# Performance work log

Measured on AMD Instinct MI355X. Metric: run time of the kernel, lower is better.

## Reference

```python
import jax, jax.numpy as jnp
import numpy as np

B, L, K, H = 256, 256, 128, 256


def setup_inputs() -> dict:
    key = jax.random.key(0)
    ks = jax.random.split(key, 24)

    def u(k, shape, fan):
        s = 1.0 / np.sqrt(fan)
        return jax.random.uniform(k, shape, minval=-s, maxval=s, dtype=jnp.float32)

    x = jax.random.normal(ks[0], (B, L, K), jnp.float32)
    mask = (jax.random.uniform(ks[1], (B, L, K)) < 0.7).astype(jnp.float32)
    record_num = jax.random.randint(ks[2], (B,), L // 2, L + 1)
    ts = jnp.cumsum(jax.random.uniform(ks[3], (B, L), minval=0.1, maxval=1.0, dtype=jnp.float32), axis=1)
    time_stamp = ts * (jnp.arange(L)[None, :] < record_num[:, None]).astype(jnp.float32)

    return {
        "x": x,
        "mask": mask,
        "time_stamp": time_stamp,
        # TemporalDecay h: W [H,K], stdv = 1/sqrt(out)=1/sqrt(H)
        "W_gh": u(ks[4], (H, K), H), "b_gh": u(ks[5], (H,), H),
        # TemporalDecay x (diag): W [K,K], stdv = 1/sqrt(K)
        "W_gx": u(ks[6], (K, K), K), "b_gx": u(ks[7], (K,), K),
        # hist_reg: Linear(H -> K), stdv = 1/sqrt(H)
        "W_hist": u(ks[8], (K, H), H), "b_hist": u(ks[9], (K,), H),
        "W_feat": u(ks[10], (K, K), K), "b_feat": u(ks[11], (K,), K),
        # weight_combine: Linear(2K -> K), stdv = 1/sqrt(2K)
        "W_comb": u(ks[12], (K, 2 * K), 2 * K), "b_comb": u(ks[13], (K,), 2 * K),
        # GRUCell(2K -> H): uniform 1/sqrt(H)
        "W_ih": u(ks[14], (3 * H, 2 * K), H), "W_hh": u(ks[15], (3 * H, H), H),
        "b_ih": u(ks[16], (3 * H,), H), "b_hh": u(ks[17], (3 * H,), H),
        # out: Linear(H -> 1)
        "W_out": u(ks[18], (1, H), H), "b_out": u(ks[19], (1,), H),
        "record_num": record_num,
        "direct": 0,
    }


def _forward(x, mask, time_stamp, W_gh, b_gh, W_gx, b_gx, W_hist, b_hist,
             W_feat, b_feat, W_comb, b_comb, W_ih, W_hh, b_ih, b_hh,
             W_out, b_out, record_num):
    Bs, Ls, Ks = x.shape
    Hs = W_gh.shape[0]
    eye = jnp.eye(Ks, dtype=x.dtype)
    W_gx_m = W_gx * eye                 # diag temporal decay
    W_feat_m = W_feat * (1.0 - eye)

    # --- deltas (gen_aux_data): d[0]=1; d[t] = |ts[t]-ts[t-1]| + (1-m[t])*d[t-1] ---
    gaps = jnp.abs(jnp.diff(time_stamp, axis=1))          # [B, L-1]
    mask_t = jnp.swapaxes(mask, 0, 1)                     # [L, B, K]

    def dstep(prev, inp):
        gap, m = inp                                      # [B], [B,K]
        d = gap[:, None] + (1.0 - m) * prev
        return d, d

    d0 = jnp.ones((Bs, Ks), x.dtype)
    _, drest = jax.lax.scan(dstep, d0, (gaps.T, mask_t[1:]))
    deltas = jnp.concatenate([d0[None], drest], axis=0)   # [L, B, K]
    valid = (jnp.arange(Ls)[:, None] < record_num[None, :])  # break at record_num
    deltas = jnp.where(valid[:, :, None], deltas, 0.0)

    evals = (time_stamp != 0).astype(x.dtype)             # [B, L]

    x_t = jnp.swapaxes(x, 0, 1)                           # [L, B, K]
    e_t = evals.T                                         # [L, B]

    def step(carry, inp):
        h, xloss = carry
        xt, mt, dt, et = inp                              # [B,K],[B,K],[B,K],[B]
        e_m = et[:, None]
        gamma_h = jnp.exp(-jax.nn.relu(dt @ W_gh.T + b_gh))   # [B,H]
        gamma_x = jnp.exp(-jax.nn.relu(dt @ W_gx_m.T + b_gx)) # [B,K]
        h_prev = h
        h = h * gamma_h
        x_h = h @ W_hist.T + b_hist
        msum = jnp.sum(mt) + 1e-5
        xloss = xloss + jnp.sum(jnp.abs(xt - x_h) * mt) / msum
        x_c = mt * xt + (1.0 - mt) * x_h
        z_h = x_c @ W_feat_m.T + b_feat
        xloss = xloss + jnp.sum(jnp.abs(xt - z_h) * mt * e_m) / msum
        alpha = jnp.concatenate([gamma_x, mt], axis=1) @ W_comb.T + b_comb
        c_h = alpha * z_h + (1.0 - alpha) * x_h
        xloss = xloss + jnp.sum(jnp.abs(xt - c_h) * mt * e_m) / msum
        c_c = mt * xt + (1.0 - mt) * c_h
        inputs = jnp.concatenate([c_c, mt], axis=1)           # [B, 2K]
        gi = inputs @ W_ih.T + b_ih                           # [B, 3H]
        gh = h @ W_hh.T + b_hh
        ir, iz, ig = jnp.split(gi, 3, axis=1)
        hr, hz, hg = jnp.split(gh, 3, axis=1)
        r = jax.nn.sigmoid(ir + hr)
        z = jax.nn.sigmoid(iz + hz)
        n = jnp.tanh(ig + r * hg)
        h_new = (1.0 - z) * n + z * h
        h_new = h_new * e_m + (1.0 - e_m) * h_prev            # freeze h past record
        return (h_new, xloss), c_c * e_m

    h0 = jnp.zeros((Bs, Hs), x.dtype)
    (h_fin, x_loss), imps = jax.lax.scan(step, (h0, jnp.float32(0.0)), (x_t, mask_t, deltas, e_t))
    imputations = jnp.swapaxes(imps, 0, 1)                # [B, L, K]
    predictions = jax.nn.sigmoid(h_fin @ W_out.T + b_out) # [B, 1]
    return imputations, x_loss, predictions


def reference(x, mask, time_stamp, W_gh, b_gh, W_gx, b_gx, W_hist, b_hist,
              W_feat, b_feat, W_comb, b_comb, W_ih, W_hh, b_ih, b_hh,
              W_out, b_out, record_num, direct):
    return _forward(x, mask, time_stamp, W_gh, b_gh, W_gx, b_gx, W_hist, b_hist,
                    W_feat, b_feat, W_comb, b_comb, W_ih, W_hh, b_ih, b_hh,
                    W_out, b_out, record_num)
```

## Files before the change

kernel.cpp:

```cpp
#include <hip/hip_runtime.h>
#include <math.h>

#define BT 256
#define LT 256
#define KT 128
#define HT 256
#define LOSS_IDX ((size_t)BT*LT*KT)
#define PRED_IDX (LOSS_IDX + 1)
#define LDP 1280
#define GH0 0
#define AL0 256
#define GI0 384
#define ZP0 1152

typedef _Float16 h2 __attribute__((ext_vector_type(2)));
typedef _Float16 f16x8 __attribute__((ext_vector_type(8)));
typedef float f32x4 __attribute__((ext_vector_type(4)));

__device__ __forceinline__ float fd2(h2 a, h2 b, float c){
#if __has_builtin(__builtin_amdgcn_fdot2)
  return __builtin_amdgcn_fdot2(a, b, c, false);
#else
  return c + (float)a[0]*(float)b[0] + (float)a[1]*(float)b[1];
#endif
}
__device__ __forceinline__ float dot8(f16x8 w, f16x8 a, float acc){
  acc = fd2(__builtin_shufflevector(w,w,0,1), __builtin_shufflevector(a,a,0,1), acc);
  acc = fd2(__builtin_shufflevector(w,w,2,3), __builtin_shufflevector(a,a,2,3), acc);
  acc = fd2(__builtin_shufflevector(w,w,4,5), __builtin_shufflevector(a,a,4,5), acc);
  acc = fd2(__builtin_shufflevector(w,w,6,7), __builtin_shufflevector(a,a,6,7), acc);
  return acc;
}
__device__ __forceinline__ float sigf(float v){ return 1.0f/(1.0f + __expf(-v)); }
__device__ __forceinline__ float tanh_fast(float v){
  float a = fminf(fabsf(v), 15.0f);
  float e2 = __expf(2.0f*a);
  float r = (e2 - 1.0f)/(e2 + 1.0f);
  return copysignf(r, v);
}
__device__ __forceinline__ float f16bits(unsigned u, int hi){
  union { unsigned short s; _Float16 h; } c;
  c.s = (unsigned short)(hi ? (u >> 16) : (u & 0xffff));
  return (float)c.h;
}

__global__ void pack_cast(const float* __restrict__ src, _Float16* __restrict__ dst,
                          int J, int Kd, int diag, int total){
  int idx = blockIdx.x*256 + threadIdx.x;
  if (idx >= total) return;
  float v = src[idx];
  if (diag && (idx / Kd) == (idx % Kd)) v = 0.0f;
  dst[idx] = (_Float16)v;
}
__global__ void pack_rowchunks(const float* __restrict__ src, _Float16* __restrict__ dst,
                               int J, int K, int total){
  int idx = blockIdx.x*256 + threadIdx.x;
  if (idx >= total) return;
  int j = idx % J, c = idx / J;
  #pragma unroll
  for (int e = 0; e < 8; ++e)
    dst[(size_t)idx*8 + e] = (_Float16)src[(size_t)j*K + c*8 + e];
}
__global__ void pack_col(const float* __restrict__ src, _Float16* __restrict__ dst,
                         int J, int Kc, int ld, int diag, int total){
  int idx = blockIdx.x*256 + threadIdx.x;
  if (idx >= total) return;
  int j = idx % J, k = idx / J;
  float v = src[(size_t)j*ld + k];
  if (diag && j == k) v = 0.0f;
  dst[idx] = (_Float16)v;
}

__global__ __launch_bounds__(128) void scan_kernel(
    const float* __restrict__ x, const float* __restrict__ mask, const float* __restrict__ ts,
    const float* __restrict__ W_gx, const float* __restrict__ b_gx,
    const int* __restrict__ record_num,
    _Float16* __restrict__ deltas, _Float16* __restrict__ Agx, _Float16* __restrict__ U)
{
  int b = blockIdx.x, k = threadIdx.x;
  int rn = record_num[b];
  float gxd = W_gx[(size_t)k*KT + k];
  float bgx = b_gx[k];
  float d = 1.0f, tsp = 0.0f;
  for (int t0 = 0; t0 < LT; t0 += 8){
    float xv[8], mv[8], tsv[8];
    #pragma unroll
    for (int u = 0; u < 8; ++u){
      size_t off = ((size_t)b*LT + t0 + u)*KT + k;
      xv[u] = x[off]; mv[u] = mask[off];
      tsv[u] = ts[(size_t)b*LT + t0 + u];
    }
    #pragma unroll
    for (int u = 0; u < 8; ++u){
      int t = t0 + u;
      if (t > 0){
        float gap = fabsf(tsv[u] - (u ? tsv[u-1] : tsp));
        d = gap + (1.0f - mv[u])*d;
      }
      float e = (t < rn) ? 1.0f : 0.0f;
      float dev = d * e;
      size_t row = (size_t)b*LT + t;
      deltas[row*KT + k] = (_Float16)dev;
      float gx = __expf(-fmaxf(fmaf(dev, gxd, bgx), 0.0f));
      Agx[row*2*KT + k]      = (_Float16)gx;
      Agx[row*2*KT + KT + k] = (_Float16)mv[u];
      U[row*2*KT + k]        = (_Float16)(mv[u]*xv[u]);
      U[row*2*KT + KT + k]   = (_Float16)mv[u];
    }
    tsp = tsv[7];
  }
}

__global__ void msum_kernel(const float* __restrict__ mask, float* __restrict__ msumInv){
  __shared__ float red[256];
  int t = blockIdx.x;
  float acc = 0.0f;
  for (int i = threadIdx.x; i < BT*KT; i += 256){
    int b = i >> 7, k = i & 127;
    acc += mask[((size_t)b*LT + t)*KT + k];
  }
  red[threadIdx.x] = acc; __syncthreads();
  for (int s = 128; s > 0; s >>= 1){
    if (threadIdx.x < s) red[threadIdx.x] += red[threadIdx.x + s];
    __syncthreads();
  }
  if (threadIdx.x == 0) msumInv[t] = 1.0f/(red[0] + 1e-5f);
}

__global__ __launch_bounds__(256) void gemm_f16(
    const _Float16* __restrict__ A, long ldA, int K,
    const _Float16* __restrict__ B, long ldB,
    _Float16* __restrict__ C, long colofs,
    const float* __restrict__ bias, int op)
{
  const int w = threadIdx.x >> 6, lane = threadIdx.x & 63;
  const int ml = lane & 15, quad = lane >> 4;
  const long m0 = (long)blockIdx.x*64 + w*16;
  const long nb0 = (long)blockIdx.y*64;
  f32x4 acc[4] = {{0,0,0,0},{0,0,0,0},{0,0,0,0},{0,0,0,0}};
  for (int kc = 0; kc < K; kc += 32){
    f16x8 a = *(const f16x8*)(A + (m0 + ml)*ldA + kc + quad*8);
    #pragma unroll
    for (int nt = 0; nt < 4; ++nt){
      f16x8 bfr = *(const f16x8*)(B + (nb0 + nt*16 + ml)*ldB + kc + quad*8);
      acc[nt] = __builtin_amdgcn_mfma_f32_16x16x32_f16(a, bfr, acc[nt], 0, 0, 0);
    }
  }
  #pragma unroll
  for (int nt = 0; nt < 4; ++nt){
    long col = nb0 + nt*16 + ml;
    float bv = (op >= 1) ? bias[col] : 0.0f;
    #pragma unroll
    for (int r = 0; r < 4; ++r){
      float v = acc[nt][r];
      if (op >= 1) v += bv;
      if (op == 2) v = __expf(-fmaxf(v, 0.0f));
      long row = m0 + quad*4 + r;
      C[row*LDP + colofs + col] = (_Float16)v;
    }
  }
}

#define NT 768

struct __align__(16) SeqS {
  f16x8 whist_l[32*128];
  _Float16 wfc_l[128*128];
  float h[HT];
  float hs[HT];
  alignas(16) _Float16 hsh[HT];
  float gh[3*HT];
  float gi[3*HT];
  float xh[KT];
  float part6[6][KT];
  float v3[KT], v5[KT];
  int lidx[136];
  int posk[KT];
  int cnt;
  unsigned pb[2][LDP/2];
  float xb[2][KT], mb[2][KT];
  float bhist[KT], bfeat[KT];
  float bhh[3*HT];
  float wout[HT];
  float minv[LT];
  float red[NT/64];
};

__global__ __launch_bounds__(NT, 1) void rits_seq(
    const float* __restrict__ x, const float* __restrict__ mask,
    const int* __restrict__ record_num, const float* __restrict__ msumInv,
    const _Float16* __restrict__ P,
    const f16x8* __restrict__ Whh_p, const f16x8* __restrict__ Whist_p,
    const _Float16* __restrict__ Wfc, const _Float16* __restrict__ Wihc,
    const float* __restrict__ b_hist, const float* __restrict__ b_feat,
    const float* __restrict__ b_hh,
    const float* __restrict__ W_out, const float* __restrict__ b_out,
    float* __restrict__ out)
{
  __shared__ SeqS s;
  const int tid = threadIdx.x;
  const int b = blockIdx.x;
  const int rn = record_num[b];
  const unsigned* __restrict__ Pd = (const unsigned*)P + (size_t)b*LT*(LDP/2);

  for (int i = tid; i < 32*128; i += NT) s.whist_l[i] = Whist_p[i];
  for (int i = tid; i < 128*128/2; i += NT)
    ((unsigned*)s.wfc_l)[i] = ((const unsigned*)Wfc)[i];
  if (tid < HT) s.h[tid] = 0.0f;
  if (tid < KT){ s.bhist[tid] = b_hist[tid]; s.bfeat[tid] = b_feat[tid]; }
  if (tid < 3*HT) s.bhh[tid] = b_hh[tid];
  if (tid < 136) s.lidx[tid] = 0;
  if (tid >= 256 && tid < 512) s.wout[tid - 256] = W_out[tid - 256];
  if (tid >= 512 && tid < 512 + LT) s.minv[tid - 512] = msumInv[tid - 512];
  if (tid < LDP/2) s.pb[0][tid] = Pd[tid];
  else if (tid < LDP/2 + KT){
    int k = tid - LDP/2;
    s.xb[0][k] = x[((size_t)b*LT)*KT + k];
    s.mb[0][k] = mask[((size_t)b*LT)*KT + k];
  }
  __syncthreads();

  float loss = 0.0f;

  for (int t = 0; t < LT; ++t){
    const int cur = t & 1, nxt = cur ^ 1;

    unsigned pr0 = 0; float prx = 0.0f, prm = 0.0f;
    if (t < LT - 1){
      if (tid < LDP/2) pr0 = Pd[(size_t)(t+1)*(LDP/2) + tid];
      else {
        int k = tid - LDP/2;
        size_t offx = ((size_t)b*LT + t + 1)*KT + k;
        prx = x[offx]; prm = mask[offx];
      }
    }
    if (tid == 0) s.cnt = 0;
    if (tid < HT){
      float g = f16bits(s.pb[cur][tid >> 1], tid & 1);
      float hsv = s.h[tid] * g;
      s.hs[tid] = hsv;
      s.hsh[tid] = (_Float16)hsv;
    }
    __syncthreads();

    {
      const f16x8* hp = (const f16x8*)s.hsh;
      if (tid < KT){
        float a2 = 0.0f;
        #pragma unroll 8
        for (int c = 0; c < 32; ++c)
          a2 = dot8(s.whist_l[c*128 + tid], hp[c], a2);
        float xh = a2 + s.bhist[tid];
        s.xh[tid] = xh;
        float mv = s.mb[cur][tid], xv = s.xb[cur][tid];
        loss += fabsf(xv - xh) * mv * s.minv[t];
        if (mv == 0.0f){
          int pp = atomicAdd(&s.cnt, 1);
          s.lidx[pp] = tid; s.v3[pp] = xh; s.posk[tid] = pp;
        }
      }
      float acc = 0.0f;
      #pragma unroll 8
      for (int c = 0; c < 32; ++c)
        acc = dot8(Whh_p[c*768 + tid], hp[c], acc);
      s.gh[tid] = acc;
    }
    __syncthreads();

    const int c0 = s.cnt;
    const int c4 = (c0 + 7) & ~7;
    {
      int st = tid >> 7, j = tid & 127;
      float a = 0.0f;
      for (int i = st; i < c0; i += 6)
        a += s.v3[i] * (float)s.wfc_l[s.lidx[i]*128 + j];
      s.part6[st][j] = a;
    }
    float wpre[16];
    #pragma unroll
    for (int u = 0; u < 16; ++u)
      wpre[u] = (u < c4) ? (float)Wihc[(size_t)s.lidx[u]*768 + tid] : 0.0f;
    __syncthreads();

    if (tid < KT){
      const int j = tid;
      if (j >= c0 && j < c4) s.v5[j] = 0.0f;
      float z = f16bits(s.pb[cur][ZP0/2 + (j >> 1)], j & 1) + s.bfeat[j]
              + s.part6[0][j] + s.part6[1][j] + s.part6[2][j]
              + s.part6[3][j] + s.part6[4][j] + s.part6[5][j];
      float al = f16bits(s.pb[cur][AL0/2 + (j >> 1)], j & 1);
      float xh = s.xh[j];
      float mv = s.mb[cur][j], xv = s.xb[cur][j];
      float e = (t < rn) ? 1.0f : 0.0f;
      float inv = s.minv[t];
      float ch = al*z + (1.0f - al)*xh;
      loss += (fabsf(xv - z) + fabsf(xv - ch)) * mv * e * inv;
      float cc = mv*xv + (1.0f - mv)*ch;
      out[((size_t)b*LT + t)*KT + j] = cc * e;
      if (mv == 0.0f) s.v5[s.posk[j]] = ch;
    }
    __syncthreads();

    {
      float g = f16bits(s.pb[cur][GI0/2 + (tid >> 1)], tid & 1);
      #pragma unroll
      for (int u = 0; u < 16; ++u)
        if (u < c4) g += s.v5[u] * wpre[u];
      for (int i = 16; i < c4; i += 8){
        #pragma unroll
        for (int u = 0; u < 8; ++u)
          g += s.v5[i + u] * (float)Wihc[(size_t)s.lidx[i + u]*768 + tid];
      }
      s.gi[tid] = g;
    }
    __syncthreads();

    if (tid < HT){
      const int j = tid;
      float ir = s.gi[j], iz = s.gi[HT + j], ig = s.gi[2*HT + j];
      float hr = s.gh[j] + s.bhh[j];
      float hz = s.gh[HT + j] + s.bhh[HT + j];
      float hg = s.gh[2*HT + j] + s.bhh[2*HT + j];
      float r = sigf(ir + hr);
      float zg = sigf(iz + hz);
      float n = tanh_fast(ig + r*hg);
      float hn = (1.0f - zg)*n + zg*s.hs[j];
      if (t < rn) s.h[j] = hn;
    }
    if (t < LT - 1){
      if (tid < LDP/2) s.pb[nxt][tid] = pr0;
      else {
        int k = tid - LDP/2;
        s.xb[nxt][k] = prx; s.mb[nxt][k] = prm;
      }
    }
    __syncthreads();
  }

  #pragma unroll
  for (int off = 32; off; off >>= 1) loss += __shfl_down(loss, off);
  if ((tid & 63) == 0) s.red[tid >> 6] = loss;
  __syncthreads();
  if (tid == 0){
    float tot = 0.0f;
    #pragma unroll
    for (int w = 0; w < NT/64; ++w) tot += s.red[w];
    atomicAdd(&out[LOSS_IDX], tot);
  }

  if (tid < HT) s.gh[tid] = s.h[tid] * s.wout[tid];
  __syncthreads();
  for (int st2 = 128; st2 > 0; st2 >>= 1){
    if (tid < st2) s.gh[tid] += s.gh[tid + st2];
    __syncthreads();
  }
  if (tid == 0) out[PRED_IDX + b] = sigf(s.gh[0] + b_out[0]);
}

extern "C" void kernel_launch(void* const* d_in, const int* in_sizes, int n_in,
                              void* d_out, int out_size, void* d_ws, size_t ws_size,
                              hipStream_t stream){
  const float* x      = (const float*)d_in[0];
  const float* mask   = (const float*)d_in[1];
  const float* ts     = (const float*)d_in[2];
  const float* W_gh   = (const float*)d_in[3];
  const float* b_gh   = (const float*)d_in[4];
  const float* W_gx   = (const float*)d_in[5];
  const float* b_gx   = (const float*)d_in[6];
  const float* W_hist = (const float*)d_in[7];
  const float* b_hist = (const float*)d_in[8];
  const float* W_feat = (const float*)d_in[9];
  const float* b_feat = (const float*)d_in[10];
  const float* W_comb = (const float*)d_in[11];
  const float* b_comb = (const float*)d_in[12];
  const float* W_ih   = (const float*)d_in[13];
  const float* W_hh   = (const float*)d_in[14];
  const float* b_ih   = (const float*)d_in[15];
  const float* b_hh   = (const float*)d_in[16];
  const float* W_out  = (const float*)d_in[17];
  const float* b_out  = (const float*)d_in[18];
  const int*   rn     = (const int*)d_in[19];
  float* out = (float*)d_out;
  char* ws = (char*)d_ws;

  size_t off = 0;
  auto alloc = [&](size_t bytes) -> char* {
    char* p = ws + off;
    off += (bytes + 255) & ~(size_t)255;
    return p;
  };
  _Float16* P      = (_Float16*)alloc((size_t)BT*LT*LDP*2);
  _Float16* deltas = (_Float16*)alloc((size_t)BT*LT*KT*2);
  _Float16* Agx    = (_Float16*)alloc((size_t)BT*LT*2*KT*2);
  _Float16* U      = (_Float16*)alloc((size_t)BT*LT*2*KT*2);
  _Float16* WghF   = (_Float16*)alloc(HT*KT*2);
  _Float16* WcombF = (_Float16*)alloc(KT*2*KT*2);
  _Float16* WihF   = (_Float16*)alloc(3*HT*2*KT*2);
  _Float16* WfeatF = (_Float16*)alloc(KT*KT*2);
  _Float16* Whh_p  = (_Float16*)alloc(3*HT*HT*2);
  _Float16* Whist_p= (_Float16*)alloc(KT*HT*2);
  _Float16* Wfc    = (_Float16*)alloc(KT*KT*2);
  _Float16* Wihc   = (_Float16*)alloc(KT*3*HT*2);
  float* msumInv   = (float*)alloc(LT*4);

  auto grid1 = [](int n){ return dim3((n + 255)/256); };
  pack_cast<<<grid1(HT*KT), 256, 0, stream>>>(W_gh, WghF, HT, KT, 0, HT*KT);
  pack_cast<<<grid1(KT*2*KT), 256, 0, stream>>>(W_comb, WcombF, KT, 2*KT, 0, KT*2*KT);
  pack_cast<<<grid1(3*HT*2*KT), 256, 0, stream>>>(W_ih, WihF, 3*HT, 2*KT, 0, 3*HT*2*KT);
  pack_cast<<<grid1(KT*KT), 256, 0, stream>>>(W_feat, WfeatF, KT, KT, 1, KT*KT);
  pack_rowchunks<<<grid1(3*HT*(HT/8)), 256, 0, stream>>>(W_hh, Whh_p, 3*HT, HT, 3*HT*(HT/8));
  pack_rowchunks<<<grid1(KT*(HT/8)), 256, 0, stream>>>(W_hist, Whist_p, KT, HT, KT*(HT/8));
  pack_col<<<grid1(KT*KT), 256, 0, stream>>>(W_feat, Wfc, KT, KT, KT, 1, KT*KT);
  pack_col<<<grid1(768*KT), 256, 0, stream>>>(W_ih, Wihc, 3*HT, KT, 2*KT, 0, 3*HT*KT);

  scan_kernel<<<dim3(BT), dim3(KT), 0, stream>>>(x, mask, ts, W_gx, b_gx, rn, deltas, Agx, U);
  msum_kernel<<<dim3(LT), dim3(256), 0, stream>>>(mask, msumInv);

  const int MR = BT*LT;
  gemm_f16<<<dim3(MR/64, HT/64), 256, 0, stream>>>(deltas, KT, KT, WghF, KT, P, GH0, b_gh, 2);
  gemm_f16<<<dim3(MR/64, KT/64), 256, 0, stream>>>(Agx, 2*KT, 2*KT, WcombF, 2*KT, P, AL0, b_comb, 1);
  gemm_f16<<<dim3(MR/64, 3*HT/64), 256, 0, stream>>>(U, 2*KT, 2*KT, WihF, 2*KT, P, GI0, b_ih, 1);
  gemm_f16<<<dim3(MR/64, KT/64), 256, 0, stream>>>(U, 2*KT, KT, WfeatF, KT, P, ZP0, (const float*)nullptr, 0);

  hipMemsetAsync((void*)(out + LOSS_IDX), 0, sizeof(float), stream);

  rits_seq<<<dim3(BT), dim3(NT), 0, stream>>>(x, mask, rn, msumInv, P,
      (const f16x8*)Whh_p, (const f16x8*)Whist_p, Wfc, Wihc,
      b_hist, b_feat, b_hh, W_out, b_out, out);
}
```

Baseline: 2.415 ms.

## Prefetch W_hh rows into registers and split dot-product accumulators

Loads most of each thread's W_hh column slice from global memory into registers at the top of each timestep, before the first barrier, so the fetch overlaps the h-scaling work. The rest is loaded after the barrier. Both the recurrent and history-regression dot products now use four independent accumulators to break the serial FMA dependency chain. The gathered W_ih loads in the input-gate loop are software-pipelined one batch ahead. The scaled hidden state stays in a register instead of shared memory. This raises register pressure, with 32 f16x8 vectors live per thread at 768 threads per block, which risks spilling or lower occupancy.

```diff
diff --git a/kernel.cpp b/kernel.cpp
--- a/kernel.cpp
+++ b/kernel.cpp
@@ -162,12 +162,13 @@
 }
 
 #define NT 768
+#define WHPRE 24
+#define WHINL (32 - WHPRE)
 
 struct __align__(16) SeqS {
   f16x8 whist_l[32*128];
   _Float16 wfc_l[128*128];
   float h[HT];
-  float hs[HT];
   alignas(16) _Float16 hsh[HT];
   float gh[3*HT];
   float gi[3*HT];
@@ -225,6 +226,9 @@
   for (int t = 0; t < LT; ++t){
     const int cur = t & 1, nxt = cur ^ 1;
 
+    f16x8 wA[WHPRE];
+    #pragma unroll
+    for (int c = 0; c < WHPRE; ++c) wA[c] = Whh_p[c*768 + tid];
     unsigned pr0 = 0; float prx = 0.0f, prm = 0.0f;
     if (t < LT - 1){
       if (tid < LDP/2) pr0 = Pd[(size_t)(t+1)*(LDP/2) + tid];
@@ -235,22 +239,45 @@
       }
     }
     if (tid == 0) s.cnt = 0;
+    float hs_r = 0.0f;
     if (tid < HT){
       float g = f16bits(s.pb[cur][tid >> 1], tid & 1);
-      float hsv = s.h[tid] * g;
-      s.hs[tid] = hsv;
-      s.hsh[tid] = (_Float16)hsv;
+      hs_r = s.h[tid] * g;
+      s.hsh[tid] = (_Float16)hs_r;
     }
     __syncthreads();
 
     {
       const f16x8* hp = (const f16x8*)s.hsh;
+      f16x8 wB[WHINL];
+      #pragma unroll
+      for (int c = 0; c < WHINL; ++c) wB[c] = Whh_p[(WHPRE + c)*768 + tid];
+      float acc0 = 0.0f, acc1 = 0.0f, acc2 = 0.0f, acc3 = 0.0f;
+      #pragma unroll
+      for (int c = 0; c < WHPRE; c += 4){
+        acc0 = dot8(wA[c],   hp[c],   acc0);
+        acc1 = dot8(wA[c+1], hp[c+1], acc1);
+        acc2 = dot8(wA[c+2], hp[c+2], acc2);
+        acc3 = dot8(wA[c+3], hp[c+3], acc3);
+      }
+      #pragma unroll
+      for (int c = 0; c < WHINL; c += 4){
+        acc0 = dot8(wB[c],   hp[WHPRE + c],   acc0);
+        acc1 = dot8(wB[c+1], hp[WHPRE + c+1], acc1);
+        acc2 = dot8(wB[c+2], hp[WHPRE + c+2], acc2);
+        acc3 = dot8(wB[c+3], hp[WHPRE + c+3], acc3);
+      }
+      s.gh[tid] = (acc0 + acc1) + (acc2 + acc3);
       if (tid < KT){
-        float a2 = 0.0f;
-        #pragma unroll 8
-        for (int c = 0; c < 32; ++c)
-          a2 = dot8(s.whist_l[c*128 + tid], hp[c], a2);
-        float xh = a2 + s.bhist[tid];
+        float a0 = 0.0f, a1 = 0.0f, a2 = 0.0f, a3 = 0.0f;
+        #pragma unroll
+        for (int c = 0; c < 32; c += 4){
+          a0 = dot8(s.whist_l[c*128 + tid],     hp[c],   a0);
+          a1 = dot8(s.whist_l[(c+1)*128 + tid], hp[c+1], a1);
+          a2 = dot8(s.whist_l[(c+2)*128 + tid], hp[c+2], a2);
+          a3 = dot8(s.whist_l[(c+3)*128 + tid], hp[c+3], a3);
+        }
+        float xh = (a0 + a1) + (a2 + a3) + s.bhist[tid];
         s.xh[tid] = xh;
         float mv = s.mb[cur][tid], xv = s.xb[cur][tid];
         loss += fabsf(xv - xh) * mv * s.minv[t];
@@ -259,11 +286,6 @@
           s.lidx[pp] = tid; s.v3[pp] = xh; s.posk[tid] = pp;
         }
       }
-      float acc = 0.0f;
-      #pragma unroll 8
-      for (int c = 0; c < 32; ++c)
-        acc = dot8(Whh_p[c*768 + tid], hp[c], acc);
-      s.gh[tid] = acc;
     }
     __syncthreads();
 
@@ -306,10 +328,24 @@
       #pragma unroll
       for (int u = 0; u < 16; ++u)
         if (u < c4) g += s.v5[u] * wpre[u];
-      for (int i = 16; i < c4; i += 8){
+      float wnx[8];
+      if (16 < c4){
         #pragma unroll
         for (int u = 0; u < 8; ++u)
-          g += s.v5[i + u] * (float)Wihc[(size_t)s.lidx[i + u]*768 + tid];
+          wnx[u] = (float)Wihc[(size_t)s.lidx[16 + u]*768 + tid];
+      }
+      for (int i = 16; i < c4; i += 8){
+        float wcu[8];
+        #pragma unroll
+        for (int u = 0; u < 8; ++u) wcu[u] = wnx[u];
+        if (i + 8 < c4){
+          #pragma unroll
+          for (int u = 0; u < 8; ++u)
+            wnx[u] = (float)Wihc[(size_t)s.lidx[i + 8 + u]*768 + tid];
+        }
+        #pragma unroll
+        for (int u = 0; u < 8; ++u)
+          g += s.v5[i + u] * wcu[u];
       }
       s.gi[tid] = g;
     }
@@ -324,7 +360,7 @@
       float r = sigf(ir + hr);
       float zg = sigf(iz + hz);
       float n = tanh_fast(ig + r*hg);
-      float hn = (1.0f - zg)*n + zg*s.hs[j];
+      float hn = (1.0f - zg)*n + zg*hs_r;
       if (t < rn) s.h[j] = hn;
     }
     if (t < LT - 1){
```

Result: slower. 4.647 ms (+92.4%).

## Process two batch sequences per workgroup to share recurrent weight loads

Applied to the files above, without the earlier changes.

Each workgroup now runs the recurrence for two batch elements at once, and the grid is halved. Each W_hh and W_hist chunk is loaded once and applied to both hidden states, halving recurrent-weight traffic per sequence. Idle thread groups now handle the second sequence's elementwise work. The cost is roughly double the per-step work on each workgroup, fewer prefetched W_ih columns (8 instead of 16 per sequence), and only half as many workgroups, which may leave many CUs unused on a 256-CU device.

```diff
diff --git a/kernel.cpp b/kernel.cpp
--- a/kernel.cpp
+++ b/kernel.cpp
@@ -166,19 +166,18 @@
 struct __align__(16) SeqS {
   f16x8 whist_l[32*128];
   _Float16 wfc_l[128*128];
-  float h[HT];
-  float hs[HT];
-  alignas(16) _Float16 hsh[HT];
-  float gh[3*HT];
-  float gi[3*HT];
-  float xh[KT];
-  float part6[6][KT];
-  float v3[KT], v5[KT];
-  int lidx[136];
-  int posk[KT];
-  int cnt;
-  unsigned pb[2][LDP/2];
-  float xb[2][KT], mb[2][KT];
+  float h0[HT], h1[HT];
+  alignas(16) _Float16 hsh0[HT], hsh1[HT];
+  float gh0[3*HT], gh1[3*HT];
+  float gi0[3*HT], gi1[3*HT];
+  float xh0[KT], xh1[KT];
+  float part0[3][KT], part1[3][KT];
+  float v30[KT], v50[KT], v31[KT], v51[KT];
+  int lidx0[136], lidx1[136];
+  int posk0[KT], posk1[KT];
+  int cnt0, cnt1;
+  unsigned pb0[2][LDP/2], pb1[2][LDP/2];
+  float xb0[2][KT], mb0[2][KT], xb1[2][KT], mb1[2][KT];
   float bhist[KT], bfeat[KT];
   float bhh[3*HT];
   float wout[HT];
@@ -199,24 +198,29 @@
 {
   __shared__ SeqS s;
   const int tid = threadIdx.x;
-  const int b = blockIdx.x;
-  const int rn = record_num[b];
-  const unsigned* __restrict__ Pd = (const unsigned*)P + (size_t)b*LT*(LDP/2);
+  const int b0 = blockIdx.x*2, b1 = b0 + 1;
+  const int rn0 = record_num[b0], rn1 = record_num[b1];
+  const unsigned* __restrict__ Pd0 = (const unsigned*)P + (size_t)b0*LT*(LDP/2);
+  const unsigned* __restrict__ Pd1 = (const unsigned*)P + (size_t)b1*LT*(LDP/2);
 
   for (int i = tid; i < 32*128; i += NT) s.whist_l[i] = Whist_p[i];
   for (int i = tid; i < 128*128/2; i += NT)
     ((unsigned*)s.wfc_l)[i] = ((const unsigned*)Wfc)[i];
-  if (tid < HT) s.h[tid] = 0.0f;
+  if (tid < HT){ s.h0[tid] = 0.0f; s.h1[tid] = 0.0f; }
   if (tid < KT){ s.bhist[tid] = b_hist[tid]; s.bfeat[tid] = b_feat[tid]; }
   if (tid < 3*HT) s.bhh[tid] = b_hh[tid];
-  if (tid < 136) s.lidx[tid] = 0;
+  if (tid < 136){ s.lidx0[tid] = 0; s.lidx1[tid] = 0; }
   if (tid >= 256 && tid < 512) s.wout[tid - 256] = W_out[tid - 256];
   if (tid >= 512 && tid < 512 + LT) s.minv[tid - 512] = msumInv[tid - 512];
-  if (tid < LDP/2) s.pb[0][tid] = Pd[tid];
-  else if (tid < LDP/2 + KT){
+  if (tid < LDP/2){
+    s.pb0[0][tid] = Pd0[tid];
+    s.pb1[0][tid] = Pd1[tid];
+  } else if (tid < LDP/2 + KT){
     int k = tid - LDP/2;
-    s.xb[0][k] = x[((size_t)b*LT)*KT + k];
-    s.mb[0][k] = mask[((size_t)b*LT)*KT + k];
+    s.xb0[0][k] = x[((size_t)b0*LT)*KT + k];
+    s.mb0[0][k] = mask[((size_t)b0*LT)*KT + k];
+    s.xb1[0][k] = x[((size_t)b1*LT)*KT + k];
+    s.mb1[0][k] = mask[((size_t)b1*LT)*KT + k];
   }
   __syncthreads();
 
@@ -225,113 +229,192 @@
   for (int t = 0; t < LT; ++t){
     const int cur = t & 1, nxt = cur ^ 1;
 
-    unsigned pr0 = 0; float prx = 0.0f, prm = 0.0f;
+    unsigned pra = 0, prb = 0;
+    float prx0 = 0.0f, prm0 = 0.0f, prx1 = 0.0f, prm1 = 0.0f;
     if (t < LT - 1){
-      if (tid < LDP/2) pr0 = Pd[(size_t)(t+1)*(LDP/2) + tid];
-      else {
+      if (tid < LDP/2){
+        pra = Pd0[(size_t)(t+1)*(LDP/2) + tid];
+        prb = Pd1[(size_t)(t+1)*(LDP/2) + tid];
+      } else {
         int k = tid - LDP/2;
-        size_t offx = ((size_t)b*LT + t + 1)*KT + k;
-        prx = x[offx]; prm = mask[offx];
-      }
-    }
-    if (tid == 0) s.cnt = 0;
+        size_t o0 = ((size_t)b0*LT + t + 1)*KT + k;
+        size_t o1 = ((size_t)b1*LT + t + 1)*KT + k;
+        prx0 = x[o0]; prm0 = mask[o0];
+        prx1 = x[o1]; prm1 = mask[o1];
+      }
+    }
+    if (tid == 0) s.cnt0 = 0;
+    if (tid == 1) s.cnt1 = 0;
+    float hs_r = 0.0f;
     if (tid < HT){
-      float g = f16bits(s.pb[cur][tid >> 1], tid & 1);
-      float hsv = s.h[tid] * g;
-      s.hs[tid] = hsv;
-      s.hsh[tid] = (_Float16)hsv;
+      float g = f16bits(s.pb0[cur][tid >> 1], tid & 1);
+      hs_r = s.h0[tid] * g;
+      s.hsh0[tid] = (_Float16)hs_r;
+    } else if (tid < 2*HT){
+      int j = tid - HT;
+      float g = f16bits(s.pb1[cur][j >> 1], j & 1);
+      hs_r = s.h1[j] * g;
+      s.hsh1[j] = (_Float16)hs_r;
     }
     __syncthreads();
 
     {
-      const f16x8* hp = (const f16x8*)s.hsh;
+      const f16x8* hp0 = (const f16x8*)s.hsh0;
+      const f16x8* hp1 = (const f16x8*)s.hsh1;
+      float g00 = 0.0f, g01 = 0.0f, g10 = 0.0f, g11 = 0.0f;
+      #pragma unroll 8
+      for (int c = 0; c < 32; c += 2){
+        f16x8 w0 = Whh_p[(size_t)c*768 + tid];
+        f16x8 w1 = Whh_p[(size_t)(c+1)*768 + tid];
+        g00 = dot8(w0, hp0[c],   g00);
+        g10 = dot8(w0, hp1[c],   g10);
+        g01 = dot8(w1, hp0[c+1], g01);
+        g11 = dot8(w1, hp1[c+1], g11);
+      }
+      s.gh0[tid] = g00 + g01;
+      s.gh1[tid] = g10 + g11;
       if (tid < KT){
-        float a2 = 0.0f;
+        float a00 = 0.0f, a01 = 0.0f, a10 = 0.0f, a11 = 0.0f;
         #pragma unroll 8
-        for (int c = 0; c < 32; ++c)
-          a2 = dot8(s.whist_l[c*128 + tid], hp[c], a2);
-        float xh = a2 + s.bhist[tid];
-        s.xh[tid] = xh;
-        float mv = s.mb[cur][tid], xv = s.xb[cur][tid];
-        loss += fabsf(xv - xh) * mv * s.minv[t];
-        if (mv == 0.0f){
-          int pp = atomicAdd(&s.cnt, 1);
-          s.lidx[pp] = tid; s.v3[pp] = xh; s.posk[tid] = pp;
+        for (int c = 0; c < 32; c += 2){
+          f16x8 w0 = s.whist_l[c*128 + tid];
+          f16x8 w1 = s.whist_l[(c+1)*128 + tid];
+          a00 = dot8(w0, hp0[c],   a00);
+          a10 = dot8(w0, hp1[c],   a10);
+          a01 = dot8(w1, hp0[c+1], a01);
+          a11 = dot8(w1, hp1[c+1], a11);
         }
-      }
-      float acc = 0.0f;
-      #pragma unroll 8
-      for (int c = 0; c < 32; ++c)
-        acc = dot8(Whh_p[c*768 + tid], hp[c], acc);
-      s.gh[tid] = acc;
-    }
-    __syncthreads();
-
-    const int c0 = s.cnt;
-    const int c4 = (c0 + 7) & ~7;
+        float xh0 = a00 + a01 + s.bhist[tid];
+        float xh1 = a10 + a11 + s.bhist[tid];
+        s.xh0[tid] = xh0; s.xh1[tid] = xh1;
+        float mv0 = s.mb0[cur][tid], xv0 = s.xb0[cur][tid];
+        float mv1 = s.mb1[cur][tid], xv1 = s.xb1[cur][tid];
+        loss += (fabsf(xv0 - xh0)*mv0 + fabsf(xv1 - xh1)*mv1) * s.minv[t];
+        if (mv0 == 0.0f){
+          int pp = atomicAdd(&s.cnt0, 1);
+          s.lidx0[pp] = tid; s.v30[pp] = xh0; s.posk0[tid] = pp;
+        }
+        if (mv1 == 0.0f){
+          int pp = atomicAdd(&s.cnt1, 1);
+          s.lidx1[pp] = tid; s.v31[pp] = xh1; s.posk1[tid] = pp;
+        }
+      }
+    }
+    __syncthreads();
+
+    const int c00 = s.cnt0, c01 = s.cnt1;
+    const int c40 = (c00 + 7) & ~7, c41 = (c01 + 7) & ~7;
     {
-      int st = tid >> 7, j = tid & 127;
-      float a = 0.0f;
-      for (int i = st; i < c0; i += 6)
-        a += s.v3[i] * (float)s.wfc_l[s.lidx[i]*128 + j];
-      s.part6[st][j] = a;
-    }
-    float wpre[16];
+      int sg = tid >> 7, j = tid & 127;
+      if (sg < 3){
+        float a = 0.0f;
+        for (int i = sg; i < c00; i += 3)
+          a += s.v30[i] * (float)s.wfc_l[s.lidx0[i]*128 + j];
+        s.part0[sg][j] = a;
+      } else {
+        int sg1 = sg - 3;
+        float a = 0.0f;
+        for (int i = sg1; i < c01; i += 3)
+          a += s.v31[i] * (float)s.wfc_l[s.lidx1[i]*128 + j];
+        s.part1[sg1][j] = a;
+      }
+    }
+    float wpre0[8], wpre1[8];
     #pragma unroll
-    for (int u = 0; u < 16; ++u)
-      wpre[u] = (u < c4) ? (float)Wihc[(size_t)s.lidx[u]*768 + tid] : 0.0f;
-    __syncthreads();
-
-    if (tid < KT){
-      const int j = tid;
-      if (j >= c0 && j < c4) s.v5[j] = 0.0f;
-      float z = f16bits(s.pb[cur][ZP0/2 + (j >> 1)], j & 1) + s.bfeat[j]
-              + s.part6[0][j] + s.part6[1][j] + s.part6[2][j]
-              + s.part6[3][j] + s.part6[4][j] + s.part6[5][j];
-      float al = f16bits(s.pb[cur][AL0/2 + (j >> 1)], j & 1);
-      float xh = s.xh[j];
-      float mv = s.mb[cur][j], xv = s.xb[cur][j];
-      float e = (t < rn) ? 1.0f : 0.0f;
-      float inv = s.minv[t];
-      float ch = al*z + (1.0f - al)*xh;
-      loss += (fabsf(xv - z) + fabsf(xv - ch)) * mv * e * inv;
-      float cc = mv*xv + (1.0f - mv)*ch;
-      out[((size_t)b*LT + t)*KT + j] = cc * e;
-      if (mv == 0.0f) s.v5[s.posk[j]] = ch;
+    for (int u = 0; u < 8; ++u){
+      wpre0[u] = (u < c40) ? (float)Wihc[(size_t)s.lidx0[u]*768 + tid] : 0.0f;
+      wpre1[u] = (u < c41) ? (float)Wihc[(size_t)s.lidx1[u]*768 + tid] : 0.0f;
+    }
+    __syncthreads();
+
+    if (tid < 2*KT){
+      const int j = tid & 127;
+      if (tid < KT){
+        if (j >= c00 && j < c40) s.v50[j] = 0.0f;
+        float z = f16bits(s.pb0[cur][ZP0/2 + (j >> 1)], j & 1) + s.bfeat[j]
+                + s.part0[0][j] + s.part0[1][j] + s.part0[2][j];
+        float al = f16bits(s.pb0[cur][AL0/2 + (j >> 1)], j & 1);
+        float xh = s.xh0[j];
+        float mv = s.mb0[cur][j], xv = s.xb0[cur][j];
+        float e = (t < rn0) ? 1.0f : 0.0f;
+        float inv = s.minv[t];
+        float ch = al*z + (1.0f - al)*xh;
+        loss += (fabsf(xv - z) + fabsf(xv - ch)) * mv * e * inv;
+        float cc = mv*xv + (1.0f - mv)*ch;
+        out[((size_t)b0*LT + t)*KT + j] = cc * e;
+        if (mv == 0.0f) s.v50[s.posk0[j]] = ch;
+      } else {
+        if (j >= c01 && j < c41) s.v51[j] = 0.0f;
+        float z = f16bits(s.pb1[cur][ZP0/2 + (j >> 1)], j & 1) + s.bfeat[j]
+                + s.part1[0][j] + s.part1[1][j] + s.part1[2][j];
+        float al = f16bits(s.pb1[cur][AL0/2 + (j >> 1)], j & 1);
+        float xh = s.xh1[j];
+        float mv = s.mb1[cur][j], xv = s.xb1[cur][j];
+        float e = (t < rn1) ? 1.0f : 0.0f;
+        float inv = s.minv[t];
+        float ch = al*z + (1.0f - al)*xh;
+        loss += (fabsf(xv - z) + fabsf(xv - ch)) * mv * e * inv;
+        float cc = mv*xv + (1.0f - mv)*ch;
+        out[((size_t)b1*LT + t)*KT + j] = cc * e;
+        if (mv == 0.0f) s.v51[s.posk1[j]] = ch;
+      }
     }
     __syncthreads();
 
     {
-      float g = f16bits(s.pb[cur][GI0/2 + (tid >> 1)], tid & 1);
+      float g0 = f16bits(s.pb0[cur][GI0/2 + (tid >> 1)], tid & 1);
+      float g1 = f16bits(s.pb1[cur][GI0/2 + (tid >> 1)], tid & 1);
       #pragma unroll
-      for (int u = 0; u < 16; ++u)
-        if (u < c4) g += s.v5[u] * wpre[u];
-      for (int i = 16; i < c4; i += 8){
+      for (int u = 0; u < 8; ++u){
+        if (u < c40) g0 += s.v50[u] * wpre0[u];
+        if (u < c41) g1 += s.v51[u] * wpre1[u];
+      }
+      for (int i = 8; i < c40; i += 8){
         #pragma unroll
         for (int u = 0; u < 8; ++u)
-          g += s.v5[i + u] * (float)Wihc[(size_t)s.lidx[i + u]*768 + tid];
-      }
-      s.gi[tid] = g;
+          g0 += s.v50[i + u] * (float)Wihc[(size_t)s.lidx0[i + u]*768 + tid];
+      }
+      for (int i = 8; i < c41; i += 8){
+        #pragma unroll
+        for (int u = 0; u < 8; ++u)
+          g1 += s.v51[i + u] * (float)Wihc[(size_t)s.lidx1[i + u]*768 + tid];
+      }
+      s.gi0[tid] = g0;
+      s.gi1[tid] = g1;
     }
     __syncthreads();
 
     if (tid < HT){
       const int j = tid;
-      float ir = s.gi[j], iz = s.gi[HT + j], ig = s.gi[2*HT + j];
-      float hr = s.gh[j] + s.bhh[j];
-      float hz = s.gh[HT + j] + s.bhh[HT + j];
-      float hg = s.gh[2*HT + j] + s.bhh[2*HT + j];
+      float ir = s.gi0[j], iz = s.gi0[HT + j], ig = s.gi0[2*HT + j];
+      float hr = s.gh0[j] + s.bhh[j];
+      float hz = s.gh0[HT + j] + s.bhh[HT + j];
+      float hg = s.gh0[2*HT + j] + s.bhh[2*HT + j];
       float r = sigf(ir + hr);
       float zg = sigf(iz + hz);
       float n = tanh_fast(ig + r*hg);
-      float hn = (1.0f - zg)*n + zg*s.hs[j];
-      if (t < rn) s.h[j] = hn;
+      float hn = (1.0f - zg)*n + zg*hs_r;
+      if (t < rn0) s.h0[j] = hn;
+    } else if (tid < 2*HT){
+      const int j = tid - HT;
+      float ir = s.gi1[j], iz = s.gi1[HT + j], ig = s.gi1[2*HT + j];
+      float hr = s.gh1[j] + s.bhh[j];
+      float hz = s.gh1[HT + j] + s.bhh[HT + j];
+      float hg = s.gh1[2*HT + j] + s.bhh[2*HT + j];
+      float r = sigf(ir + hr);
+      float zg = sigf(iz + hz);
+      float n = tanh_fast(ig + r*hg);
+      float hn = (1.0f - zg)*n + zg*hs_r;
+      if (t < rn1) s.h1[j] = hn;
     }
     if (t < LT - 1){
-      if (tid < LDP/2) s.pb[nxt][tid] = pr0;
-      else {
+      if (tid < LDP/2){
+        s.pb0[nxt][tid] = pra;
+        s.pb1[nxt][tid] = prb;
+      } else {
         int k = tid - LDP/2;
-        s.xb[nxt][k] = prx; s.mb[nxt][k] = prm;
+        s.xb0[nxt][k] = prx0; s.mb0[nxt][k] = prm0;
+        s.xb1[nxt][k] = prx1; s.mb1[nxt][k] = prm1;
       }
     }
     __syncthreads();
@@ -348,13 +431,16 @@
     atomicAdd(&out[LOSS_IDX], tot);
   }
 
-  if (tid < HT) s.gh[tid] = s.h[tid] * s.wout[tid];
+  if (tid < HT) s.gh0[tid] = s.h0[tid] * s.wout[tid];
+  else if (tid < 2*HT) s.gh1[tid - HT] = s.h1[tid - HT] * s.wout[tid - HT];
   __syncthreads();
   for (int st2 = 128; st2 > 0; st2 >>= 1){
-    if (tid < st2) s.gh[tid] += s.gh[tid + st2];
-    __syncthreads();
-  }
-  if (tid == 0) out[PRED_IDX + b] = sigf(s.gh[0] + b_out[0]);
+    if (tid < st2) s.gh0[tid] += s.gh0[tid + st2];
+    else if (tid >= 256 && tid < 256 + st2) s.gh1[tid - 256] += s.gh1[tid - 256 + st2];
+    __syncthreads();
+  }
+  if (tid == 0)   out[PRED_IDX + b0] = sigf(s.gh0[0] + b_out[0]);
+  if (tid == 256) out[PRED_IDX + b1] = sigf(s.gh1[0] + b_out[0]);
 }
 
 extern "C" void kernel_launch(void* const* d_in, const int* in_sizes, int n_in,
@@ -424,7 +510,7 @@
 
   hipMemsetAsync((void*)(out + LOSS_IDX), 0, sizeof(float), stream);
 
-  rits_seq<<<dim3(BT), dim3(NT), 0, stream>>>(x, mask, rn, msumInv, P,
+  rits_seq<<<dim3(BT/2), dim3(NT), 0, stream>>>(x, mask, rn, msumInv, P,
       (const f16x8*)Whh_p, (const f16x8*)Whist_p, Wfc, Wihc,
       b_hist, b_feat, b_hh, W_out, b_out, out);
 }
```

New measurement: 3.735 ms. 1.55x slower.

## Cut per-step barriers by overlapping recurrent matvec with feature regression and fusing GRU input

Applied to the files above, without the earlier changes.

Reorganizes each recurrence step from six barriers to three. The hidden state now lives in registers, and the next step's decayed hidden state is produced inside the GRU stage. The W_hh matvec runs on threads 128+ while threads 0–127 do the feature regression and imputation. The masked input-gate accumulation is folded into the GRU update, and the global prefetch now uses the worker threads. The goal is to shorten the latency-bound serial loop, at the cost of more work and register pressure per thread and unbalanced thread roles.

```diff
diff --git a/kernel.cpp b/kernel.cpp
--- a/kernel.cpp
+++ b/kernel.cpp
@@ -166,17 +166,13 @@
 struct __align__(16) SeqS {
   f16x8 whist_l[32*128];
   _Float16 wfc_l[128*128];
-  float h[HT];
-  float hs[HT];
   alignas(16) _Float16 hsh[HT];
   float gh[3*HT];
-  float gi[3*HT];
   float xh[KT];
-  float part6[6][KT];
   float v3[KT], v5[KT];
   int lidx[136];
   int posk[KT];
-  int cnt;
+  int cnt[2];
   unsigned pb[2][LDP/2];
   float xb[2][KT], mb[2][KT];
   float bhist[KT], bfeat[KT];
@@ -206,10 +202,11 @@
   for (int i = tid; i < 32*128; i += NT) s.whist_l[i] = Whist_p[i];
   for (int i = tid; i < 128*128/2; i += NT)
     ((unsigned*)s.wfc_l)[i] = ((const unsigned*)Wfc)[i];
-  if (tid < HT) s.h[tid] = 0.0f;
-  if (tid < KT){ s.bhist[tid] = b_hist[tid]; s.bfeat[tid] = b_feat[tid]; }
+  if (tid < KT){ s.bhist[tid] = b_hist[tid]; s.bfeat[tid] = b_feat[tid]; s.v3[tid] = 0.0f; }
   if (tid < 3*HT) s.bhh[tid] = b_hh[tid];
   if (tid < 136) s.lidx[tid] = 0;
+  if (tid < HT) s.hsh[tid] = (_Float16)0.0f;
+  if (tid == 0){ s.cnt[0] = 0; s.cnt[1] = 0; }
   if (tid >= 256 && tid < 512) s.wout[tid - 256] = W_out[tid - 256];
   if (tid >= 512 && tid < 512 + LT) s.minv[tid - 512] = msumInv[tid - 512];
   if (tid < LDP/2) s.pb[0][tid] = Pd[tid];
@@ -221,118 +218,129 @@
   __syncthreads();
 
   float loss = 0.0f;
+  float h_reg = 0.0f;
+  float hs_r = 0.0f;
 
   for (int t = 0; t < LT; ++t){
     const int cur = t & 1, nxt = cur ^ 1;
 
     unsigned pr0 = 0; float prx = 0.0f, prm = 0.0f;
-    if (t < LT - 1){
-      if (tid < LDP/2) pr0 = Pd[(size_t)(t+1)*(LDP/2) + tid];
-      else {
-        int k = tid - LDP/2;
-        size_t offx = ((size_t)b*LT + t + 1)*KT + k;
-        prx = x[offx]; prm = mask[offx];
-      }
-    }
-    if (tid == 0) s.cnt = 0;
-    if (tid < HT){
-      float g = f16bits(s.pb[cur][tid >> 1], tid & 1);
-      float hsv = s.h[tid] * g;
-      s.hs[tid] = hsv;
-      s.hsh[tid] = (_Float16)hsv;
+    if (t < LT - 1 && tid >= 128){
+      pr0 = Pd[(size_t)(t+1)*(LDP/2) + (tid - 128)];
+      if (tid < 256){
+        int k = tid - 128;
+        size_t o = ((size_t)b*LT + t + 1)*KT + k;
+        prx = x[o]; prm = mask[o];
+      }
+    }
+    if (tid == 0) s.cnt[nxt] = 0;
+    if (tid < KT){
+      const f16x8* hp = (const f16x8*)s.hsh;
+      float b0 = 0.0f, b1 = 0.0f, b2 = 0.0f, b3 = 0.0f;
+      #pragma unroll 8
+      for (int c = 0; c < 32; c += 4){
+        b0 = dot8(s.whist_l[c*128 + tid],     hp[c],   b0);
+        b1 = dot8(s.whist_l[(c+1)*128 + tid], hp[c+1], b1);
+        b2 = dot8(s.whist_l[(c+2)*128 + tid], hp[c+2], b2);
+        b3 = dot8(s.whist_l[(c+3)*128 + tid], hp[c+3], b3);
+      }
+      float xh = (b0 + b1) + (b2 + b3) + s.bhist[tid];
+      s.xh[tid] = xh;
+      float mv = s.mb[cur][tid];
+      if (mv == 0.0f){
+        int pp = atomicAdd(&s.cnt[cur], 1);
+        s.lidx[pp] = tid; s.v3[pp] = xh; s.posk[tid] = pp;
+      }
     }
     __syncthreads();
 
-    {
+    const int c0 = s.cnt[cur];
+    const int c4 = (c0 + 7) & ~7;
+    if (tid >= 128){
       const f16x8* hp = (const f16x8*)s.hsh;
-      if (tid < KT){
-        float a2 = 0.0f;
+      {
+        const int o = tid - 128;
+        float a0 = 0.0f, a1 = 0.0f, a2 = 0.0f, a3 = 0.0f;
         #pragma unroll 8
-        for (int c = 0; c < 32; ++c)
-          a2 = dot8(s.whist_l[c*128 + tid], hp[c], a2);
-        float xh = a2 + s.bhist[tid];
-        s.xh[tid] = xh;
-        float mv = s.mb[cur][tid], xv = s.xb[cur][tid];
-        loss += fabsf(xv - xh) * mv * s.minv[t];
-        if (mv == 0.0f){
-          int pp = atomicAdd(&s.cnt, 1);
-          s.lidx[pp] = tid; s.v3[pp] = xh; s.posk[tid] = pp;
+        for (int c = 0; c < 32; c += 4){
+          a0 = dot8(Whh_p[(size_t)c*768 + o],     hp[c],   a0);
+          a1 = dot8(Whh_p[(size_t)(c+1)*768 + o], hp[c+1], a1);
+          a2 = dot8(Whh_p[(size_t)(c+2)*768 + o], hp[c+2], a2);
+          a3 = dot8(Whh_p[(size_t)(c+3)*768 + o], hp[c+3], a3);
         }
-      }
-      float acc = 0.0f;
-      #pragma unroll 8
-      for (int c = 0; c < 32; ++c)
-        acc = dot8(Whh_p[c*768 + tid], hp[c], acc);
-      s.gh[tid] = acc;
-    }
-    __syncthreads();
-
-    const int c0 = s.cnt;
-    const int c4 = (c0 + 7) & ~7;
-    {
-      int st = tid >> 7, j = tid & 127;
-      float a = 0.0f;
-      for (int i = st; i < c0; i += 6)
-        a += s.v3[i] * (float)s.wfc_l[s.lidx[i]*128 + j];
-      s.part6[st][j] = a;
-    }
-    float wpre[16];
-    #pragma unroll
-    for (int u = 0; u < 16; ++u)
-      wpre[u] = (u < c4) ? (float)Wihc[(size_t)s.lidx[u]*768 + tid] : 0.0f;
-    __syncthreads();
-
-    if (tid < KT){
+        s.gh[o] = (a0 + a1) + (a2 + a3);
+      }
+      if (tid >= 256 && tid < 384){
+        const int o = tid + 384;
+        float a0 = 0.0f, a1 = 0.0f, a2 = 0.0f, a3 = 0.0f;
+        #pragma unroll 8
+        for (int c = 0; c < 32; c += 4){
+          a0 = dot8(Whh_p[(size_t)c*768 + o],     hp[c],   a0);
+          a1 = dot8(Whh_p[(size_t)(c+1)*768 + o], hp[c+1], a1);
+          a2 = dot8(Whh_p[(size_t)(c+2)*768 + o], hp[c+2], a2);
+          a3 = dot8(Whh_p[(size_t)(c+3)*768 + o], hp[c+3], a3);
+        }
+        s.gh[o] = (a0 + a1) + (a2 + a3);
+      }
+      if (t < LT - 1){
+        s.pb[nxt][tid - 128] = pr0;
+        if (tid < 256){
+          int k = tid - 128;
+          s.xb[nxt][k] = prx; s.mb[nxt][k] = prm;
+        }
+      }
+    } else {
       const int j = tid;
-      if (j >= c0 && j < c4) s.v5[j] = 0.0f;
-      float z = f16bits(s.pb[cur][ZP0/2 + (j >> 1)], j & 1) + s.bfeat[j]
-              + s.part6[0][j] + s.part6[1][j] + s.part6[2][j]
-              + s.part6[3][j] + s.part6[4][j] + s.part6[5][j];
+      float z0 = 0.0f, z1 = 0.0f;
+      for (int i = 0; i < c4; i += 2){
+        z0 += s.v3[i]   * (float)s.wfc_l[s.lidx[i]*128 + j];
+        z1 += s.v3[i+1] * (float)s.wfc_l[s.lidx[i+1]*128 + j];
+      }
+      float z  = f16bits(s.pb[cur][ZP0/2 + (j >> 1)], j & 1) + s.bfeat[j] + z0 + z1;
       float al = f16bits(s.pb[cur][AL0/2 + (j >> 1)], j & 1);
       float xh = s.xh[j];
       float mv = s.mb[cur][j], xv = s.xb[cur][j];
-      float e = (t < rn) ? 1.0f : 0.0f;
+      float e  = (t < rn) ? 1.0f : 0.0f;
       float inv = s.minv[t];
       float ch = al*z + (1.0f - al)*xh;
-      loss += (fabsf(xv - z) + fabsf(xv - ch)) * mv * e * inv;
+      loss += (fabsf(xv - xh) + (fabsf(xv - z) + fabsf(xv - ch))*e) * mv * inv;
       float cc = mv*xv + (1.0f - mv)*ch;
       out[((size_t)b*LT + t)*KT + j] = cc * e;
+      if (j >= c0) s.v5[j] = 0.0f;
       if (mv == 0.0f) s.v5[s.posk[j]] = ch;
-    }
-    __syncthreads();
-
-    {
-      float g = f16bits(s.pb[cur][GI0/2 + (tid >> 1)], tid & 1);
-      #pragma unroll
-      for (int u = 0; u < 16; ++u)
-        if (u < c4) g += s.v5[u] * wpre[u];
-      for (int i = 16; i < c4; i += 8){
-        #pragma unroll
-        for (int u = 0; u < 8; ++u)
-          g += s.v5[i + u] * (float)Wihc[(size_t)s.lidx[i + u]*768 + tid];
-      }
-      s.gi[tid] = g;
     }
     __syncthreads();
 
     if (tid < HT){
       const int j = tid;
-      float ir = s.gi[j], iz = s.gi[HT + j], ig = s.gi[2*HT + j];
-      float hr = s.gh[j] + s.bhh[j];
-      float hz = s.gh[HT + j] + s.bhh[HT + j];
+      float gr = f16bits(s.pb[cur][GI0/2        + (j >> 1)], j & 1);
+      float gz = f16bits(s.pb[cur][(GI0+HT)/2   + (j >> 1)], j & 1);
+      float gg = f16bits(s.pb[cur][(GI0+2*HT)/2 + (j >> 1)], j & 1);
+      for (int i = 0; i < c4; i += 8){
+        #pragma unroll
+        for (int u = 0; u < 8; ++u){
+          int li = s.lidx[i + u];
+          float v = s.v5[i + u];
+          gr += v * (float)Wihc[(size_t)li*768 + j];
+          gz += v * (float)Wihc[(size_t)li*768 + 256 + j];
+          gg += v * (float)Wihc[(size_t)li*768 + 512 + j];
+        }
+      }
+      float hr = s.gh[j]        + s.bhh[j];
+      float hz = s.gh[HT + j]   + s.bhh[HT + j];
       float hg = s.gh[2*HT + j] + s.bhh[2*HT + j];
-      float r = sigf(ir + hr);
-      float zg = sigf(iz + hz);
-      float n = tanh_fast(ig + r*hg);
-      float hn = (1.0f - zg)*n + zg*s.hs[j];
-      if (t < rn) s.h[j] = hn;
-    }
-    if (t < LT - 1){
-      if (tid < LDP/2) s.pb[nxt][tid] = pr0;
-      else {
-        int k = tid - LDP/2;
-        s.xb[nxt][k] = prx; s.mb[nxt][k] = prm;
-      }
+      float r  = sigf(gr + hr);
+      float zg = sigf(gz + hz);
+      float n  = tanh_fast(gg + r*hg);
+      float hn = (1.0f - zg)*n + zg*hs_r;
+      if (t < rn) h_reg = hn;
+      if (t < LT - 1){
+        float g = f16bits(s.pb[nxt][j >> 1], j & 1);
+        hs_r = h_reg * g;
+        s.hsh[j] = (_Float16)hs_r;
+      }
+    } else if (tid < HT + KT){
+      s.v3[tid - HT] = 0.0f;
     }
     __syncthreads();
   }
@@ -348,7 +356,7 @@
     atomicAdd(&out[LOSS_IDX], tot);
   }
 
-  if (tid < HT) s.gh[tid] = s.h[tid] * s.wout[tid];
+  if (tid < HT) s.gh[tid] = h_reg * s.wout[tid];
   __syncthreads();
   for (int st2 = 128; st2 > 0; st2 >>= 1){
     if (tid < st2) s.gh[tid] += s.gh[tid + st2];
```

New measurement: 4.313 ms. 78.6% more time.
